# Performance work log

Hardware: AMD Instinct MI355X
Metric: run time of the kernel (lower is better)

Reference implementation:

```python
import jax, jax.numpy as jnp
import numpy as np

W = 128
POS_FREQ = 10  # -> 3*10*2 = 60 encoded dims
VIEW_FREQ = 4  # -> 3*4*2 = 24 encoded dims


def freq_encode(v, n_freq):
    # tcnn 'Frequency' encoding: sin/cos of 2^j * pi * x per input dim.
    scales = (2.0 ** jnp.arange(n_freq, dtype=v.dtype)) * jnp.pi  # [F]
    ang = v[..., :, None] * scales  # [N, 3, F]
    enc = jnp.stack([jnp.sin(ang), jnp.cos(ang)], axis=-1)  # [N, 3, F, 2]
    return enc.reshape(v.shape[0], -1)  # [N, 3*F*2]


def mlp(h, weights):
    # tcnn FullyFusedMLP: bias-free, ReLU on hidden layers, linear output.
    for Wm in weights[:-1]:
        h = jax.nn.relu(h @ Wm)
    return h @ weights[-1]


def setup_inputs():
    key = jax.random.key(0)
    ks = jax.random.split(key, 10)
    N = 1048576

    def w(k, fan_in, fan_out):
        s = (1.0 / np.sqrt(fan_in)).astype(np.float32)
        return jax.random.uniform(k, (fan_in, fan_out), jnp.float32, -s, s)

    return {
        "x": jax.random.uniform(ks[0], (N, 6), jnp.float32),
        "Wd1_0": w(ks[1], 60, W),
        "Wd1_1": w(ks[2], W, W),
        "Wd1_2": w(ks[3], W, W),
        "Wd2_0": w(ks[4], 60 + W, W),
        "Wd2_1": w(ks[5], W, W),
        "Wd2_2": w(ks[6], W, W),
        "Wd2_3": w(ks[7], W, W + 1),
        "Wc_0": w(ks[8], 24 + W, W),
        "Wc_1": w(ks[9], W, 3),
    }


def reference(x, Wd1_0, Wd1_1, Wd1_2, Wd2_0, Wd2_1, Wd2_2, Wd2_3, Wc_0, Wc_1):
    pos, view = x[:, :3], x[:, 3:6]
    # Density MLP
    enc_pos = freq_encode(pos, POS_FREQ)                # [N, 60]
    part1 = mlp(enc_pos, [Wd1_0, Wd1_1, Wd1_2])          # [N, 128]
    dens_out = mlp(jnp.concatenate([enc_pos, part1], -1),
                   [Wd2_0, Wd2_1, Wd2_2, Wd2_3])         # [N, 129]
    blending = jax.nn.sigmoid(dens_out[:, :1])           # [N, 1]
    feature = dens_out[:, 1:]                            # [N, 128]
    density = feature[:, 0:1]                            # [N, 1]
    # Color MLP
    enc_view = freq_encode(view, VIEW_FREQ)              # [N, 24]
    rgb = mlp(jnp.concatenate([enc_view, feature], -1), [Wc_0, Wc_1])  # [N, 3]
    return jnp.concatenate([rgb, density, blending], -1)  # [N, 5]
```

## Files before the change

### kernel.cpp

```cpp
#include <hip/hip_runtime.h>
#include <cstdint>
#include <cstddef>

typedef __attribute__((ext_vector_type(8))) __bf16 bf16x8;
typedef __attribute__((ext_vector_type(16))) float floatx16;

struct SrcPtrs { const float* p[9]; };


__global__ void prep_zero(unsigned short* __restrict__ ws) {
  uint4* p = (uint4*)ws;
  const int n = 143360 / 8;
  for (int i = blockIdx.x * blockDim.x + threadIdx.x; i < n; i += gridDim.x * blockDim.x)
    p[i] = make_uint4(0u, 0u, 0u, 0u);
}

__global__ void prep_fill(SrcPtrs sp, unsigned short* __restrict__ ws) {
  const int m  = blockIdx.x >> 4;
  const int sl = blockIdx.x & 15;
  const int K[9]  = {60, 128, 128, 188, 128, 128, 128, 152, 128};
  const int N[9]  = {128, 128, 128, 128, 128, 128, 129, 128, 3};
  const int SS[9] = {4, 8, 8, 12, 8, 8, 8, 10, 8};
  const unsigned OFF[9] = {0u, 8192u, 24576u, 40960u, 65536u, 81920u, 98304u, 118784u, 139264u};
  const int Km = K[m], Nm = N[m], Sm = SS[m];
  const float* __restrict__ src = sp.p[m];
  unsigned short* __restrict__ dst = ws + OFF[m];
  const int tot = Km * Nm;
  for (int i = sl * 256 + (int)threadIdx.x; i < tot; i += 16 * 256) {
    int k = i / Nm;
    int n = i - k * Nm;
    int kk = k, row = n;
    if (m == 3) kk = (k < 60) ? 128 + k : k - 60;
    if (m == 7) kk = (k < 24) ? 128 + k : k - 24;
    if (m == 6) row = (n == 0) ? 128 : n - 1;
    const int t = row >> 5, l31 = row & 31;
    const int s = kk >> 4, q2 = (kk >> 3) & 1, j = kk & 7;
    dst[(t * Sm + s) * 512 + (q2 * 32 + l31) * 8 + j] =
        __builtin_bit_cast(unsigned short, (__bf16)src[i]);
  }
}


#if defined(__has_builtin)
#if __has_builtin(__builtin_amdgcn_permlane32_swap)
#define HAVE_PLSWAP 1
#endif
#endif
#ifndef HAVE_PLSWAP
#define HAVE_PLSWAP 0
#endif

__device__ __forceinline__ unsigned pk2(float a, float b) {
  unsigned short ua = __builtin_bit_cast(unsigned short, (__bf16)a);
  unsigned short ub = __builtin_bit_cast(unsigned short, (__bf16)b);
  return (unsigned)ua | ((unsigned)ub << 16);
}

__device__ __forceinline__ void stage16(const void* g, void* l) {
  __builtin_amdgcn_global_load_lds(
      (const __attribute__((address_space(1))) unsigned int*)g,
      (__attribute__((address_space(3))) unsigned int*)l, 16, 0, 0);
}

__device__ __forceinline__ void half_swap(unsigned a, unsigned b, int q2,
                                          unsigned& lo, unsigned& hi) {
#if HAVE_PLSWAP
  auto r = __builtin_amdgcn_permlane32_swap(a, b, false, false);
  lo = r[0]; hi = r[1];
#else
  unsigned sa = __shfl_xor(a, 32, 64);
  unsigned sb = __shfl_xor(b, 32, 64);
  lo = q2 ? sb : a;
  hi = q2 ? b : sa;
#endif
}

template <int KIND>
__device__ __forceinline__ bf16x8 trig_frag(const float (&x)[6], int q2, int sl) {
  bf16x8 r;
#pragma unroll
  for (int j = 0; j < 8; ++j) {
    const int kA = 16 * sl + j;
    const int kB = 16 * sl + 8 + j;
    int dA, dB; float scA, scB; bool vA, vB;
    if (KIND == 0) {
      vA = kA < 60; vB = kB < 60;
      dA = kA / 20; dB = kB / 20;
      scA = (float)(1 << ((kA % 20) >> 1)) * 0.5f;
      scB = (float)(1 << ((kB % 20) >> 1)) * 0.5f;
    } else {
      vA = kA < 24; vB = kB < 24;
      dA = 3 + (kA >> 3); dB = 3 + (kB >> 3);
      scA = (float)(1 << ((kA & 7) >> 1)) * 0.5f;
      scB = (float)(1 << ((kB & 7) >> 1)) * 0.5f;
    }
    float v  = q2 ? x[dB] : x[dA];
    float sc = q2 ? scB : scA;
    bool ok  = q2 ? vB : vA;
    float rev = v * sc;
    float t = (j & 1) ? __builtin_amdgcn_cosf(rev) : __builtin_amdgcn_sinf(rev);
    r[j] = (__bf16)(ok ? t : 0.0f);
  }
  return r;
}

template <int S, int SL, int NT, int HT, int PP, bool RELU, int OUTM>
__device__ __forceinline__ void run_layer(const unsigned short* __restrict__ wsrc,
                                          const unsigned short* __restrict__ nsrc, int nbytes,
                                          unsigned short* __restrict__ sWt,
                                          uint2 (&pkv)[16],
                                          const bf16x8 (&tail)[4],
                                          float* __restrict__ out, int base, int tid) {
  const int lane = tid & 63;
  const int w = tid >> 6;
  const int q2 = lane >> 5;
  const int l31 = lane & 31;
  const int pt0 = base + w * 32 + l31;

  __syncthreads();

  if (nbytes > 0) {
    const uint4* __restrict__ s4 = (const uint4*)nsrc;
    uint4* __restrict__ dst = (uint4*)(sWt + (PP ^ 1) * 8192);
    const int n16 = nbytes / 16;
    for (int i = tid; i < n16; i += 256)
      stage16(s4 + i, dst + (i & ~63));
  }

  bf16x8 bf[SL > 0 ? SL : 1];
#pragma unroll
  for (int s = 0; s < SL; ++s) {
    uint2 p0 = pkv[2 * s], p1 = pkv[2 * s + 1];
    unsigned w0, w1, w2, w3;
    half_swap(p0.x, p1.x, q2, w0, w2);
    half_swap(p0.y, p1.y, q2, w1, w3);
    uint4 u = make_uint4(w0, w1, w2, w3);
    bf[s] = __builtin_bit_cast(bf16x8, u);
  }

  const unsigned short* __restrict__ ldsbuf = sWt + PP * 8192;
  const uint4* __restrict__ wp = (const uint4*)wsrc;
#pragma unroll
  for (int t = 0; t < NT; ++t) {
    floatx16 acc;
#pragma unroll
    for (int i = 0; i < 16; ++i) acc[i] = 0.0f;
#pragma unroll
    for (int s = 0; s < S; ++s) {
      bf16x8 A;
      if (t < HT) {
        A = *(const bf16x8*)&ldsbuf[(t * S + s) * 512 + lane * 8];
      } else {
        uint4 a4 = wp[(t * S + s) * 64 + lane];
        A = __builtin_bit_cast(bf16x8, a4);
      }
      bf16x8 B0 = (s < SL) ? bf[s < SL ? s : 0] : tail[s - SL];
      acc = __builtin_amdgcn_mfma_f32_32x32x16_bf16(A, B0, acc, 0, 0, 0);
    }
    if (OUTM == 2) {
      if (q2 == 0) {
        float* o0 = out + (size_t)pt0 * 5;
        o0[0] = acc[0]; o0[1] = acc[1]; o0[2] = acc[2];
      }
    } else {
      if (OUTM == 0 || t < 4) {
#pragma unroll
        for (int gg = 0; gg < 4; ++gg) {
          float b0 = acc[4 * gg], b1 = acc[4 * gg + 1];
          float b2 = acc[4 * gg + 2], b3 = acc[4 * gg + 3];
          if (RELU) {
            b0 = fmaxf(b0, 0.f); b1 = fmaxf(b1, 0.f);
            b2 = fmaxf(b2, 0.f); b3 = fmaxf(b3, 0.f);
          }
          pkv[4 * t + gg] = make_uint2(pk2(b0, b1), pk2(b2, b3));
        }
      }
      if (OUTM == 1 && q2 == 0) {
        if (t == 0) {
          out[(size_t)pt0 * 5 + 3] = acc[0];
        }
        if (t == 4) {
          out[(size_t)pt0 * 5 + 4] = 1.0f / (1.0f + __expf(-acc[0]));
        }
      }
    }
  }
}

__global__ __launch_bounds__(256, 3) void nerf_main(const float* __restrict__ x,
                                                    const unsigned short* __restrict__ ws,
                                                    float* __restrict__ out) {
  __shared__ __align__(16) unsigned short sWt[2 * 8192];

  const int tid = (int)threadIdx.x;
  const int base = (int)blockIdx.x * 128;
  const int lane = tid & 63;
  const int w = tid >> 6;
  const int q2 = lane >> 5;
  const int l31 = lane & 31;
  const int pt0 = base + w * 32 + l31;

  {
    const uint4* s4 = (const uint4*)ws;
    uint4* dst = (uint4*)sWt;
#pragma unroll
    for (int i = 0; i < 4; ++i)
      stage16(s4 + i * 256 + tid, dst + ((i * 256 + tid) & ~63));
  }

  float x0[6];
  {
    const float* a = x + (size_t)pt0 * 6;
#pragma unroll
    for (int c = 0; c < 3; ++c) {
      float2 u = *(const float2*)(a + 2 * c);
      x0[2 * c] = u.x; x0[2 * c + 1] = u.y;
    }
  }

  bf16x8 pkt[4];
#pragma unroll
  for (int sl = 0; sl < 4; ++sl)
    pkt[sl] = trig_frag<0>(x0, q2, sl);

  uint2 pkv[16];

  run_layer< 4, 0, 4, 4, 0, true , 0>(ws + 0u,      ws + 8192u,   16384, sWt, pkv, pkt, out, base, tid);
  run_layer< 8, 8, 4, 2, 1, true , 0>(ws + 8192u,   ws + 24576u,  16384, sWt, pkv, pkt, out, base, tid);
  run_layer< 8, 8, 4, 2, 0, false, 0>(ws + 24576u,  ws + 40960u,  12288, sWt, pkv, pkt, out, base, tid);
  run_layer<12, 8, 4, 1, 1, true , 0>(ws + 40960u,  ws + 65536u,  16384, sWt, pkv, pkt, out, base, tid);
  run_layer< 8, 8, 4, 2, 0, true , 0>(ws + 65536u,  ws + 81920u,  16384, sWt, pkv, pkt, out, base, tid);
  run_layer< 8, 8, 4, 2, 1, true , 0>(ws + 81920u,  ws + 98304u,  16384, sWt, pkv, pkt, out, base, tid);
  run_layer< 8, 8, 5, 2, 0, false, 1>(ws + 98304u,  ws + 118784u, 10240, sWt, pkv, pkt, out, base, tid);

  bf16x8 vw[4];
#pragma unroll
  for (int sl = 0; sl < 2; ++sl)
    vw[sl] = trig_frag<1>(x0, q2, sl);
  vw[2] = vw[0]; vw[3] = vw[0];

  run_layer<10, 8, 4, 1, 1, true , 0>(ws + 118784u, ws + 139264u,  8192, sWt, pkv, vw,  out, base, tid);
  run_layer< 8, 8, 1, 1, 0, false, 2>(ws + 139264u, (const unsigned short*)nullptr, 0, sWt, pkv, pkt, out, base, tid);
}

extern "C" void kernel_launch(void* const* d_in, const int* in_sizes, int n_in,
                              void* d_out, int out_size, void* d_ws, size_t ws_size,
                              hipStream_t stream) {
  (void)n_in; (void)out_size; (void)ws_size;
  const float* x = (const float*)d_in[0];
  SrcPtrs sp;
  for (int i = 0; i < 9; ++i) sp.p[i] = (const float*)d_in[1 + i];
  unsigned short* ws = (unsigned short*)d_ws;
  float* out = (float*)d_out;
  const int N = in_sizes[0] / 6;

  prep_zero<<<70, 256, 0, stream>>>(ws);
  prep_fill<<<144, 256, 0, stream>>>(sp, ws);
  nerf_main<<<N / 128, 256, 0, stream>>>(x, ws, out);
}
```

Baseline: 400.3 us.

## Process multiple point chunks per block with runtime-parameterized mid layers

Each block now processes four 128-point chunks in a loop, and the first layer's weights for the next chunk are prefetched during the last layer. Four same-shaped middle layers are collapsed into one non-unrolled loop, with weight offsets, ping-pong buffer and ReLU limit read from device constant tables. This shrinks code size and register pressure, which lets launch bounds ask for 4 waves per SIMD, and it amortizes per-block startup. In exchange, table loads and runtime buffer indexing add overhead, and the grid holds a quarter as many blocks.

```diff
diff --git a/kernel.cpp b/kernel.cpp
--- a/kernel.cpp
+++ b/kernel.cpp
@@ -104,9 +104,10 @@
   return r;
 }
 
-template <int S, int SL, int NT, int HT, int PP, bool RELU, int OUTM>
+template <int S, int SL, int NT, int HT, int OUTM>
 __device__ __forceinline__ void run_layer(const unsigned short* __restrict__ wsrc,
                                           const unsigned short* __restrict__ nsrc, int nbytes,
+                                          int pp, float relu_lim,
                                           unsigned short* __restrict__ sWt,
                                           uint2 (&pkv)[16],
                                           const bf16x8 (&tail)[4],
@@ -121,7 +122,7 @@
 
   if (nbytes > 0) {
     const uint4* __restrict__ s4 = (const uint4*)nsrc;
-    uint4* __restrict__ dst = (uint4*)(sWt + (PP ^ 1) * 8192);
+    uint4* __restrict__ dst = (uint4*)(sWt + (pp ^ 1) * 8192);
     const int n16 = nbytes / 16;
     for (int i = tid; i < n16; i += 256)
       stage16(s4 + i, dst + (i & ~63));
@@ -138,7 +139,7 @@
     bf[s] = __builtin_bit_cast(bf16x8, u);
   }
 
-  const unsigned short* __restrict__ ldsbuf = sWt + PP * 8192;
+  const unsigned short* __restrict__ ldsbuf = sWt + pp * 8192;
   const uint4* __restrict__ wp = (const uint4*)wsrc;
 #pragma unroll
   for (int t = 0; t < NT; ++t) {
@@ -166,12 +167,10 @@
       if (OUTM == 0 || t < 4) {
 #pragma unroll
         for (int gg = 0; gg < 4; ++gg) {
-          float b0 = acc[4 * gg], b1 = acc[4 * gg + 1];
-          float b2 = acc[4 * gg + 2], b3 = acc[4 * gg + 3];
-          if (RELU) {
-            b0 = fmaxf(b0, 0.f); b1 = fmaxf(b1, 0.f);
-            b2 = fmaxf(b2, 0.f); b3 = fmaxf(b3, 0.f);
-          }
+          float b0 = fmaxf(acc[4 * gg], relu_lim);
+          float b1 = fmaxf(acc[4 * gg + 1], relu_lim);
+          float b2 = fmaxf(acc[4 * gg + 2], relu_lim);
+          float b3 = fmaxf(acc[4 * gg + 3], relu_lim);
           pkv[4 * t + gg] = make_uint2(pk2(b0, b1), pk2(b2, b3));
         }
       }
@@ -187,18 +186,25 @@
   }
 }
 
-__global__ __launch_bounds__(256, 3) void nerf_main(const float* __restrict__ x,
+__device__ const unsigned g_mid_wo[4]  = {8192u, 24576u, 65536u, 81920u};
+__device__ const unsigned g_mid_no[4]  = {24576u, 40960u, 81920u, 98304u};
+__device__ const int      g_mid_nb[4]  = {16384, 12288, 16384, 16384};
+__device__ const int      g_mid_ppb[4] = {1, 0, 0, 1};
+__device__ const float    g_mid_lim[4] = {0.0f, -__builtin_inff(), 0.0f, 0.0f};
+
+#define CHUNKS 4
+
+__global__ __launch_bounds__(256, 4) void nerf_main(const float* __restrict__ x,
                                                     const unsigned short* __restrict__ ws,
                                                     float* __restrict__ out) {
   __shared__ __align__(16) unsigned short sWt[2 * 8192];
 
   const int tid = (int)threadIdx.x;
-  const int base = (int)blockIdx.x * 128;
   const int lane = tid & 63;
   const int w = tid >> 6;
   const int q2 = lane >> 5;
   const int l31 = lane & 31;
-  const int pt0 = base + w * 32 + l31;
+  const float NINF = -__builtin_inff();
 
   {
     const uint4* s4 = (const uint4*)ws;
@@ -208,39 +214,61 @@
       stage16(s4 + i * 256 + tid, dst + ((i * 256 + tid) & ~63));
   }
 
-  float x0[6];
-  {
-    const float* a = x + (size_t)pt0 * 6;
-#pragma unroll
-    for (int c = 0; c < 3; ++c) {
-      float2 u = *(const float2*)(a + 2 * c);
-      x0[2 * c] = u.x; x0[2 * c + 1] = u.y;
-    }
-  }
-
-  bf16x8 pkt[4];
-#pragma unroll
-  for (int sl = 0; sl < 4; ++sl)
-    pkt[sl] = trig_frag<0>(x0, q2, sl);
-
-  uint2 pkv[16];
-
-  run_layer< 4, 0, 4, 4, 0, true , 0>(ws + 0u,      ws + 8192u,   16384, sWt, pkv, pkt, out, base, tid);
-  run_layer< 8, 8, 4, 2, 1, true , 0>(ws + 8192u,   ws + 24576u,  16384, sWt, pkv, pkt, out, base, tid);
-  run_layer< 8, 8, 4, 2, 0, false, 0>(ws + 24576u,  ws + 40960u,  12288, sWt, pkv, pkt, out, base, tid);
-  run_layer<12, 8, 4, 1, 1, true , 0>(ws + 40960u,  ws + 65536u,  16384, sWt, pkv, pkt, out, base, tid);
-  run_layer< 8, 8, 4, 2, 0, true , 0>(ws + 65536u,  ws + 81920u,  16384, sWt, pkv, pkt, out, base, tid);
-  run_layer< 8, 8, 4, 2, 1, true , 0>(ws + 81920u,  ws + 98304u,  16384, sWt, pkv, pkt, out, base, tid);
-  run_layer< 8, 8, 5, 2, 0, false, 1>(ws + 98304u,  ws + 118784u, 10240, sWt, pkv, pkt, out, base, tid);
-
-  bf16x8 vw[4];
-#pragma unroll
-  for (int sl = 0; sl < 2; ++sl)
-    vw[sl] = trig_frag<1>(x0, q2, sl);
-  vw[2] = vw[0]; vw[3] = vw[0];
-
-  run_layer<10, 8, 4, 1, 1, true , 0>(ws + 118784u, ws + 139264u,  8192, sWt, pkv, vw,  out, base, tid);
-  run_layer< 8, 8, 1, 1, 0, false, 2>(ws + 139264u, (const unsigned short*)nullptr, 0, sWt, pkv, pkt, out, base, tid);
+  int p0 = 0;
+
+#pragma unroll 1
+  for (int c = 0; c < CHUNKS; ++c) {
+    const int base = ((int)blockIdx.x * CHUNKS + c) * 128;
+    const int pt0 = base + w * 32 + l31;
+
+    float x0[6];
+    {
+      const float* a = x + (size_t)pt0 * 6;
+#pragma unroll
+      for (int cc = 0; cc < 3; ++cc) {
+        float2 u = *(const float2*)(a + 2 * cc);
+        x0[2 * cc] = u.x; x0[2 * cc + 1] = u.y;
+      }
+    }
+
+    bf16x8 pkt[4];
+#pragma unroll
+    for (int sl = 0; sl < 4; ++sl)
+      pkt[sl] = trig_frag<0>(x0, q2, sl);
+
+    uint2 pkv[16];
+
+    run_layer<4, 0, 4, 4, 0>(ws + 0u, ws + 8192u, 16384, p0, 0.0f,
+                             sWt, pkv, pkt, out, base, tid);
+
+#pragma unroll 1
+    for (int i = 0; i < 4; ++i) {
+      run_layer<8, 8, 4, 2, 0>(ws + g_mid_wo[i], ws + g_mid_no[i], g_mid_nb[i],
+                               p0 ^ g_mid_ppb[i], g_mid_lim[i],
+                               sWt, pkv, pkt, out, base, tid);
+      if (i == 1)
+        run_layer<12, 8, 4, 1, 0>(ws + 40960u, ws + 65536u, 16384, p0 ^ 1, 0.0f,
+                                  sWt, pkv, pkt, out, base, tid);
+    }
+
+    run_layer<8, 8, 5, 2, 1>(ws + 98304u, ws + 118784u, 10240, p0, NINF,
+                             sWt, pkv, pkt, out, base, tid);
+
+    bf16x8 vw[4];
+#pragma unroll
+    for (int sl = 0; sl < 2; ++sl)
+      vw[sl] = trig_frag<1>(x0, q2, sl);
+    vw[2] = vw[0]; vw[3] = vw[0];
+
+    run_layer<10, 8, 4, 1, 0>(ws + 118784u, ws + 139264u, 8192, p0 ^ 1, 0.0f,
+                              sWt, pkv, vw, out, base, tid);
+
+    const int nb_next = (c == CHUNKS - 1) ? 0 : 16384;
+    run_layer<8, 8, 1, 1, 2>(ws + 139264u, ws, nb_next, p0, NINF,
+                             sWt, pkv, pkt, out, base, tid);
+
+    p0 ^= 1;
+  }
 }
 
 extern "C" void kernel_launch(void* const* d_in, const int* in_sizes, int n_in,
@@ -256,5 +284,5 @@
 
   prep_zero<<<70, 256, 0, stream>>>(ws);
   prep_fill<<<144, 256, 0, stream>>>(sp, ws);
-  nerf_main<<<N / 128, 256, 0, stream>>>(x, ws, out);
-}
+  nerf_main<<<N / (128 * CHUNKS), 256, 0, stream>>>(x, ws, out);
+}
```

Result: slower. 1.121 ms (+180.1%).
